# Kernel optimization log

Hardware: AMD Instinct MI355X
Metric: run time of the kernel (lower is better)

Reference implementation:

```python
import jax, jax.numpy as jnp
import numpy as np

BATCH, NODES, CH_IN, CH_OUT, N_EXPERTS = 8, 8192, 128, 128, 64

def setup_inputs() -> dict:
    key = jax.random.key(0)
    kx, kw, ks = jax.random.split(key, 3)
    x = jax.random.normal(kx, (BATCH, NODES, CH_IN), dtype=jnp.float32)
    # std = fan_in**-0.5 per self_init
    W = jax.random.normal(kw, (N_EXPERTS, CH_OUT, CH_IN), dtype=jnp.float32) * (CH_IN ** -0.5)
    sel = jax.random.randint(ks, (NODES,), 0, N_EXPERTS, dtype=jnp.int64)
    return {"x": x, "sel": sel, "W": W}

def reference(x, sel, W):
    # x: (b, n, j), W[sel]: (n, i, j) -> out: (b, n, i)
    Wsel = W[sel]  # gather a (ch_out, ch_in) matrix per node
    return jnp.einsum('bnj,nij->bni', x, Wsel)
```

## Files before the change

kernel.cpp:

```cpp
#include <hip/hip_runtime.h>
#include <hip/hip_bf16.h>

#define BATCH   8
#define NODES   8192
#define CH      128
#define NEXP    64
#define TN      16
#define MAXP    (NODES + NEXP * TN)
#define NTILES  (MAXP / TN)

typedef __attribute__((ext_vector_type(8))) short bf16x8;
typedef __attribute__((ext_vector_type(4))) float f32x4;

__device__ __forceinline__ short f2bf(float f) {
    union { float f; unsigned u; } v; v.f = f;
    unsigned r = (v.u + 0x7fffu + ((v.u >> 16) & 1u)) >> 16;
    return (short)r;
}

__device__ __forceinline__ bf16x8 cvt8(f32x4 lo, f32x4 hi) {
    bf16x8 r;
    r[0] = f2bf(lo[0]); r[1] = f2bf(lo[1]); r[2] = f2bf(lo[2]); r[3] = f2bf(lo[3]);
    r[4] = f2bf(hi[0]); r[5] = f2bf(hi[1]); r[6] = f2bf(hi[2]); r[7] = f2bf(hi[3]);
    return r;
}

__global__ __launch_bounds__(1024)
void sort_kernel(const int* __restrict__ sel, int* __restrict__ sorted)
{
    __shared__ int cnt[NEXP];
    __shared__ int cur[NEXP];
    const int t = threadIdx.x;

    if (t < NEXP) cnt[t] = 0;
    __syncthreads();

    int mye[NODES / 1024];
    #pragma unroll
    for (int i = 0; i < NODES / 1024; ++i) {
        mye[i] = sel[i * 1024 + t];
        atomicAdd(&cnt[mye[i]], 1);
    }
    __syncthreads();

    if (t == 0) {
        int off = 0;
        for (int e = 0; e < NEXP; ++e) {
            cur[e] = off;
            off += (cnt[e] + TN - 1) & ~(TN - 1);
        }
    }
    __syncthreads();

    for (int i = t; i < MAXP; i += 1024) sorted[i] = -1;
    __syncthreads();

    #pragma unroll
    for (int i = 0; i < NODES / 1024; ++i) {
        int pos = atomicAdd(&cur[mye[i]], 1);
        sorted[pos] = i * 1024 + t;
    }
}

__global__ __launch_bounds__(256)
void gemm_kernel(const float* __restrict__ x, const int* __restrict__ sel,
                 const float* __restrict__ W, float* __restrict__ out,
                 const int* __restrict__ sorted)
{
    __shared__ int s_nodes[TN];
    __shared__ int s_expert;

    const int tid  = threadIdx.x;
    const int tile = blockIdx.x;

    if (tid < TN) s_nodes[tid] = sorted[tile * TN + tid];
    if (tid == 0) {
        int n0 = sorted[tile * TN];
        s_expert = (n0 >= 0) ? sel[n0] : -1;
    }
    __syncthreads();

    const int e = s_expert;
    if (e < 0) return;

    const int wave = tid >> 6;
    const int lane = tid & 63;
    const int m16  = lane & 15;
    const int quad = lane >> 4;

    const float* xrow[2];
    #pragma unroll
    for (int rt = 0; rt < 2; ++rt) {
        int r    = wave * 32 + rt * 16 + m16;
        int node = s_nodes[r >> 3];
        int b    = r & 7;
        int nd   = (node >= 0) ? node : 0;
        xrow[rt] = x + ((size_t)(b * NODES + nd)) * CH;
    }
    const float* wbase = W + (size_t)e * CH * CH;

    f32x4 acc[2][8];
    #pragma unroll
    for (int rt = 0; rt < 2; ++rt)
        #pragma unroll
        for (int ct = 0; ct < 8; ++ct)
            acc[rt][ct] = (f32x4){0.f, 0.f, 0.f, 0.f};

    #pragma unroll
    for (int kk = 0; kk < 4; ++kk) {
        const int k0 = kk * 32 + quad * 8;

        bf16x8 afrag[2];
        #pragma unroll
        for (int rt = 0; rt < 2; ++rt) {
            const float* p = xrow[rt] + k0;
            f32x4 lo = *reinterpret_cast<const f32x4*>(p);
            f32x4 hi = *reinterpret_cast<const f32x4*>(p + 4);
            afrag[rt] = cvt8(lo, hi);
        }

        #pragma unroll
        for (int ct = 0; ct < 8; ++ct) {
            const float* p = wbase + (size_t)(ct * 16 + m16) * CH + k0;
            f32x4 lo = *reinterpret_cast<const f32x4*>(p);
            f32x4 hi = *reinterpret_cast<const f32x4*>(p + 4);
            bf16x8 bfrag = cvt8(lo, hi);
            acc[0][ct] = __builtin_amdgcn_mfma_f32_16x16x32_bf16(
                             afrag[0], bfrag, acc[0][ct], 0, 0, 0);
            acc[1][ct] = __builtin_amdgcn_mfma_f32_16x16x32_bf16(
                             afrag[1], bfrag, acc[1][ct], 0, 0, 0);
        }
    }

    #pragma unroll
    for (int rt = 0; rt < 2; ++rt) {
        #pragma unroll
        for (int reg = 0; reg < 4; ++reg) {
            int r    = wave * 32 + rt * 16 + quad * 4 + reg;
            int node = s_nodes[r >> 3];
            if (node < 0) continue;
            int b = r & 7;
            float* orow = out + ((size_t)(b * NODES + node)) * CH;
            #pragma unroll
            for (int ct = 0; ct < 8; ++ct)
                orow[ct * 16 + m16] = acc[rt][ct][reg];
        }
    }
}

extern "C" void kernel_launch(void* const* d_in, const int* in_sizes, int n_in,
                              void* d_out, int out_size, void* d_ws, size_t ws_size,
                              hipStream_t stream)
{
    const float* x   = (const float*)d_in[0];
    const int*   sel = (const int*)  d_in[1];
    const float* W   = (const float*)d_in[2];
    float*       out = (float*)d_out;
    int*      sorted = (int*)d_ws;

    sort_kernel<<<1, 1024, 0, stream>>>(sel, sorted);
    gemm_kernel<<<NTILES, 256, 0, stream>>>(x, sel, W, out, sorted);
}
```

Baseline: 116.0 us.

## Pre-convert expert weights to bf16 and parallelize sort across per-expert blocks

Replaces the single-block sort kernel with a 64-block prep kernel. Each block converts one expert's weight matrix to bf16 in workspace, then builds that expert's segment of the sorted node list. The gemm kernel then loads bf16 weights directly instead of reloading and converting fp32 weights in every tile, which halves weight traffic and drops the conversion ALU work. In exchange, every block redundantly histograms all of sel, and the weight conversion runs on each call.

```diff
diff --git a/kernel.cpp b/kernel.cpp
--- a/kernel.cpp
+++ b/kernel.cpp
@@ -25,46 +25,71 @@
     return r;
 }
 
-__global__ __launch_bounds__(1024)
-void sort_kernel(const int* __restrict__ sel, int* __restrict__ sorted)
+__global__ __launch_bounds__(256)
+void prep_kernel(const int* __restrict__ sel, const float* __restrict__ W,
+                 short* __restrict__ Wbf, int* __restrict__ sorted)
 {
-    __shared__ int cnt[NEXP];
-    __shared__ int cur[NEXP];
+    const int e = blockIdx.x;
     const int t = threadIdx.x;
 
+    {
+        const float* ws = W   + (size_t)e * CH * CH;
+        short*       wd = Wbf + (size_t)e * CH * CH;
+        #pragma unroll
+        for (int i = 0; i < 8; ++i) {
+            int idx = (i * 256 + t) * 8;
+            f32x4 lo = *reinterpret_cast<const f32x4*>(ws + idx);
+            f32x4 hi = *reinterpret_cast<const f32x4*>(ws + idx + 4);
+            *reinterpret_cast<bf16x8*>(wd + idx) = cvt8(lo, hi);
+        }
+    }
+
+    __shared__ int cnt[NEXP];
+    __shared__ int s_off, s_cnt, cursor;
     if (t < NEXP) cnt[t] = 0;
+    if (t == 0) cursor = 0;
     __syncthreads();
 
-    int mye[NODES / 1024];
+    int myv[NODES / 256];
     #pragma unroll
-    for (int i = 0; i < NODES / 1024; ++i) {
-        mye[i] = sel[i * 1024 + t];
-        atomicAdd(&cnt[mye[i]], 1);
+    for (int i = 0; i < NODES / 256; ++i) {
+        myv[i] = sel[i * 256 + t];
+        atomicAdd(&cnt[myv[i]], 1);
     }
     __syncthreads();
 
     if (t == 0) {
-        int off = 0;
-        for (int e = 0; e < NEXP; ++e) {
-            cur[e] = off;
-            off += (cnt[e] + TN - 1) & ~(TN - 1);
+        int off = 0, myoff = 0;
+        for (int ee = 0; ee < NEXP; ++ee) {
+            if (ee == e) myoff = off;
+            off += (cnt[ee] + TN - 1) & ~(TN - 1);
         }
+        s_off = myoff;
+        s_cnt = cnt[e];
     }
     __syncthreads();
 
-    for (int i = t; i < MAXP; i += 1024) sorted[i] = -1;
-    __syncthreads();
+    const int off = s_off, myc = s_cnt;
+    const int pad = (myc + TN - 1) & ~(TN - 1);
+
+    for (int i = myc + t; i < pad; i += 256) sorted[off + i] = -1;
+
+    if (e == NEXP - 1) {
+        for (int i = off + pad + t; i < MAXP; i += 256) sorted[i] = -1;
+    }
 
     #pragma unroll
-    for (int i = 0; i < NODES / 1024; ++i) {
-        int pos = atomicAdd(&cur[mye[i]], 1);
-        sorted[pos] = i * 1024 + t;
+    for (int i = 0; i < NODES / 256; ++i) {
+        if (myv[i] == e) {
+            int pos = atomicAdd(&cursor, 1);
+            sorted[off + pos] = i * 256 + t;
+        }
     }
 }
 
 __global__ __launch_bounds__(256)
 void gemm_kernel(const float* __restrict__ x, const int* __restrict__ sel,
-                 const float* __restrict__ W, float* __restrict__ out,
+                 const short* __restrict__ Wbf, float* __restrict__ out,
                  const int* __restrict__ sorted)
 {
     __shared__ int s_nodes[TN];
@@ -97,7 +122,7 @@
         int nd   = (node >= 0) ? node : 0;
         xrow[rt] = x + ((size_t)(b * NODES + nd)) * CH;
     }
-    const float* wbase = W + (size_t)e * CH * CH;
+    const short* wbase = Wbf + (size_t)e * CH * CH;
 
     f32x4 acc[2][8];
     #pragma unroll
@@ -121,10 +146,8 @@
 
         #pragma unroll
         for (int ct = 0; ct < 8; ++ct) {
-            const float* p = wbase + (size_t)(ct * 16 + m16) * CH + k0;
-            f32x4 lo = *reinterpret_cast<const f32x4*>(p);
-            f32x4 hi = *reinterpret_cast<const f32x4*>(p + 4);
-            bf16x8 bfrag = cvt8(lo, hi);
+            bf16x8 bfrag = *reinterpret_cast<const bf16x8*>(
+                wbase + (size_t)(ct * 16 + m16) * CH + k0);
             acc[0][ct] = __builtin_amdgcn_mfma_f32_16x16x32_bf16(
                              afrag[0], bfrag, acc[0][ct], 0, 0, 0);
             acc[1][ct] = __builtin_amdgcn_mfma_f32_16x16x32_bf16(
@@ -156,8 +179,10 @@
     const int*   sel = (const int*)  d_in[1];
     const float* W   = (const float*)d_in[2];
     float*       out = (float*)d_out;
-    int*      sorted = (int*)d_ws;
 
-    sort_kernel<<<1, 1024, 0, stream>>>(sel, sorted);
-    gemm_kernel<<<NTILES, 256, 0, stream>>>(x, sel, W, out, sorted);
+    short* Wbf   = (short*)d_ws;
+    int*   sorted = (int*)((char*)d_ws + (size_t)NEXP * CH * CH * sizeof(short));
+
+    prep_kernel<<<NEXP, 256, 0, stream>>>(sel, W, Wbf, sorted);
+    gemm_kernel<<<NTILES, 256, 0, stream>>>(x, sel, Wbf, out, sorted);
 }
```

New measurement: 115.5 us. Within noise of the previous version (-0.4%).
